# Optimization experiments

Hardware: AMD Instinct MI355X
Metric: run time of the kernel (lower is better)

## Reference

```python
import jax, jax.numpy as jnp
import numpy as np

B, C, H, N = 2, 128, 128, 2048   # batch, in_channels, hidden_dim, points per view
TEMP = 0.1
ITERS = 20
EPS = 1e-8


def setup_inputs() -> dict:
    key = jax.random.key(0)
    ks = jax.random.split(key, 4)
    s = lambda fan_in: 1.0 / np.sqrt(fan_in)
    return {
        "feat_d": jax.random.normal(ks[0], (B, C, N), jnp.float32),
        "feat_s": jax.random.normal(ks[1], (B, C, N), jnp.float32),
        # dustbin_head params: Conv1d(C->H, k=1) -> ReLU -> Conv1d(H->1, k=1)
        "W1": jax.random.normal(ks[2], (H, C), jnp.float32) * s(C),
        "b1": jnp.zeros((H,), jnp.float32),
        "W2": jax.random.normal(ks[3], (1, H), jnp.float32) * s(H),
        "b2": jnp.zeros((1,), jnp.float32),
    }


def _dustbin_head(x, W1, b1, W2, b2):
    # 1x1 Conv1d == channel matmul. x: [B, C, N] -> [B, 1, N]
    h = jax.nn.relu(jnp.einsum('hc,bcn->bhn', W1, x) + b1[None, :, None])
    return jnp.einsum('oh,bhn->bon', W2, h) + b2[None, :, None]


def _log_cross_view_ot(feat_q, feat_k, dustbin, temperature, iters):
    # scores: [B, Nq, Nk]; dustbin appended as the last row -> [B, Nq+1, Nk]
    scores = jnp.einsum('bcn,bcm->bnm', feat_q, feat_k) / temperature
    log_T0 = jnp.concatenate([scores, dustbin], axis=1)

    def step(log_T, _):
        log_T = log_T - jax.nn.logsumexp(log_T, axis=2, keepdims=True)  # row norm
        log_T = log_T - jax.nn.logsumexp(log_T, axis=1, keepdims=True)  # col norm
        return log_T, None

    log_T, _ = jax.lax.scan(step, log_T0, None, length=iters)
    return log_T


def reference(feat_d, feat_s, W1, b1, W2, b2):
    # N_d == N_s, so the torch F.interpolate calls are identity ops.
    dust_d = _dustbin_head(feat_d, W1, b1, W2, b2)  # [B, 1, N]
    dust_s = _dustbin_head(feat_s, W1, b1, W2, b2)  # [B, 1, N]

    log_T_ds = _log_cross_view_ot(feat_d, feat_s, dust_d, TEMP, ITERS)
    log_T_sd = _log_cross_view_ot(feat_s, feat_d, dust_s, TEMP, ITERS)

    T_ds = jnp.exp(log_T_ds[:, :-1, :])  # drop dustbin row -> [B, N, N]
    T_sd = jnp.exp(log_T_sd[:, :-1, :])

    loss_consistency = jnp.mean((T_ds - jnp.swapaxes(T_sd, 1, 2)) ** 2)

    entropy_ds = -(T_ds * jnp.log(T_ds + EPS)).sum(axis=(1, 2)).mean()
    entropy_sd = -(T_sd * jnp.log(T_sd + EPS)).sum(axis=(1, 2)).mean()
    loss_entropy = 0.5 * (entropy_ds + entropy_sd)

    return loss_consistency + 0.01 * loss_entropy
```

## Files before the change

kernel.cpp:

```cpp
#include <hip/hip_runtime.h>
#include <hip/hip_fp16.h>
#include <math.h>

#define NPTS 2048
#define NB 2
#define NC 128
#define NH 128
#define INV_TEMP 10.0f
#define NITERS 20
#define EPSF 1e-8f

static __device__ __forceinline__ void lse_merge(float& m, float& s, float m2, float s2){
  float M = fmaxf(m, m2);
  s = s * __expf(m - M) + s2 * __expf(m2 - M);
  m = M;
}

static __device__ __forceinline__ void unpack8(uint4 raw, float* x){
  float2 f;
  f = __half22float2(*(__half2*)&raw.x); x[0]=f.x; x[1]=f.y;
  f = __half22float2(*(((__half2*)&raw.x)+1)); x[2]=f.x; x[3]=f.y;
  f = __half22float2(*(__half2*)&raw.z); x[4]=f.x; x[5]=f.y;
  f = __half22float2(*(((__half2*)&raw.z)+1)); x[6]=f.x; x[7]=f.y;
}

static __device__ __forceinline__ float reduce32_lse(float* x){
  float m = x[0];
  #pragma unroll
  for (int i = 1; i < 32; ++i) m = fmaxf(m, x[i]);
  float s = 0.f;
  #pragma unroll
  for (int i = 0; i < 32; ++i) s += __expf(x[i] - m);
  #pragma unroll
  for (int d = 1; d < 64; d <<= 1){
    float m2 = __shfl_xor(m, d);
    float s2 = __shfl_xor(s, d);
    lse_merge(m, s, m2, s2);
  }
  return m + __logf(s);
}

__global__ __launch_bounds__(128) void dust_kernel(
    const float* __restrict__ fd, const float* __restrict__ fs,
    const float* __restrict__ W1, const float* __restrict__ b1,
    const float* __restrict__ W2, const float* __restrict__ b2,
    float* __restrict__ dust_d, float* __restrict__ dust_s){
  const int chunk = blockIdx.x, b = blockIdx.y, view = blockIdx.z;
  const float* x = (view == 0 ? fd : fs) + (size_t)b * NC * NPTS;
  float* out = (view == 0 ? dust_d : dust_s) + (size_t)b * NPTS;
  const int n0 = chunk * 16;
  __shared__ float xs[NC][17];
  __shared__ float red[NH][17];
  const int j = threadIdx.x;
  #pragma unroll
  for (int p = 0; p < 16; ++p) xs[j][p] = x[(size_t)j * NPTS + n0 + p];
  __syncthreads();
  float acc[16];
  float bb = b1[j];
  #pragma unroll
  for (int p = 0; p < 16; ++p) acc[p] = bb;
  for (int c = 0; c < NC; ++c){
    float w = W1[j * NC + c];
    #pragma unroll
    for (int p = 0; p < 16; ++p) acc[p] = fmaf(w, xs[c][p], acc[p]);
  }
  float w2 = W2[j];
  #pragma unroll
  for (int p = 0; p < 16; ++p) red[j][p] = w2 * fmaxf(acc[p], 0.0f);
  __syncthreads();
  for (int s = NH / 2; s >= 1; s >>= 1){
    if (j < s){
      #pragma unroll
      for (int p = 0; p < 16; ++p) red[j][p] += red[j + s][p];
    }
    __syncthreads();
  }
  if (j < 16) out[n0 + j] = red[0][j] + b2[0];
}

#define GP 68
__global__ __launch_bounds__(256) void gemm_kernel(
    const float* __restrict__ fd, const float* __restrict__ fs,
    __half* __restrict__ S, __half* __restrict__ ST){
  const int cb = blockIdx.x, rb = blockIdx.y, b = blockIdx.z;
  const float* A = fd + (size_t)b * NC * NPTS;
  const float* Bm = fs + (size_t)b * NC * NPTS;
  __shared__ float Als[NC * GP];
  __shared__ float Bls[NC * GP];
  const int tid = threadIdx.x;
  for (int idx = tid; idx < NC * 64; idx += 256){
    int ch = idx >> 6, i = idx & 63;
    Als[ch * GP + i] = A[(size_t)ch * NPTS + rb * 64 + i];
    Bls[ch * GP + i] = Bm[(size_t)ch * NPTS + cb * 64 + i];
  }
  __syncthreads();
  const int tx = tid & 15, ty = tid >> 4;
  float acc[4][4] = {};
  for (int c = 0; c < NC; ++c){
    float4 a4 = *(const float4*)&Als[c * GP + ty * 4];
    float4 b4 = *(const float4*)&Bls[c * GP + tx * 4];
    float av[4] = {a4.x, a4.y, a4.z, a4.w};
    float bv[4] = {b4.x, b4.y, b4.z, b4.w};
    #pragma unroll
    for (int i = 0; i < 4; ++i)
      #pragma unroll
      for (int jj = 0; jj < 4; ++jj)
        acc[i][jj] = fmaf(av[i], bv[jj], acc[i][jj]);
  }
  __half* Sb = S + (size_t)b * NPTS * NPTS;
  __half* STb = ST + (size_t)b * NPTS * NPTS;
  const int r0 = rb * 64 + ty * 4, c0 = cb * 64 + tx * 4;
  #pragma unroll
  for (int i = 0; i < 4; ++i){
    __half2 p[2];
    p[0] = __float22half2_rn(make_float2(acc[i][0]*INV_TEMP, acc[i][1]*INV_TEMP));
    p[1] = __float22half2_rn(make_float2(acc[i][2]*INV_TEMP, acc[i][3]*INV_TEMP));
    *(uint2*)&Sb[(size_t)(r0 + i) * NPTS + c0] = *(uint2*)p;
  }
  #pragma unroll
  for (int jj = 0; jj < 4; ++jj){
    __half2 p[2];
    p[0] = __float22half2_rn(make_float2(acc[0][jj]*INV_TEMP, acc[1][jj]*INV_TEMP));
    p[1] = __float22half2_rn(make_float2(acc[2][jj]*INV_TEMP, acc[3][jj]*INV_TEMP));
    *(uint2*)&STb[(size_t)(c0 + jj) * NPTS + r0] = *(uint2*)p;
  }
}

__global__ __launch_bounds__(512, 4) void phase_kernel(
    const __half* __restrict__ S, const __half* __restrict__ ST,
    const float* __restrict__ dust_d, const float* __restrict__ dust_s,
    float* __restrict__ u_ds, float* __restrict__ u_sd,
    float* __restrict__ v_ds, float* __restrict__ v_sd,
    const int mode){
  const int b = blockIdx.y, mat = blockIdx.z;
  const int w = threadIdx.x >> 6, lane = threadIdx.x & 63;
  const int r = blockIdx.x * 8 + w;
  const int rmax = (mode == 0) ? (NPTS + 1) : NPTS;

  __shared__ float lds_off[NPTS];
  {
    const float* off;
    if (mode == 0) off = (mat == 0 ? v_ds : v_sd) + b * NPTS;
    else           off = (mat == 0 ? u_sd : u_ds) + b * (NPTS + 1);
    *(float4*)&lds_off[threadIdx.x * 4] = *(const float4*)&off[threadIdx.x * 4];
  }
  __syncthreads();

  if (r >= rmax) return;

  float x[32];
  if (mode == 0 && r == NPTS){
    const float* drow = (mat == 0 ? dust_d : dust_s) + b * NPTS;
    #pragma unroll
    for (int k = 0; k < 8; ++k){
      const int c = (k * 64 + lane) * 4;
      float4 rv = *(const float4*)&drow[c];
      float4 o  = *(const float4*)&lds_off[c];
      x[k*4+0]=rv.x+o.x; x[k*4+1]=rv.y+o.y; x[k*4+2]=rv.z+o.z; x[k*4+3]=rv.w+o.w;
    }
  } else {
    const __half* row = ((mode == 0) == (mat == 0) ? S : ST);
    row = (mat == 0 ? S : ST);
    row += ((size_t)b * NPTS + r) * NPTS;
    #pragma unroll
    for (int k2 = 0; k2 < 4; ++k2){
      const int c = (k2 * 64 + lane) * 8;
      uint4 raw = *(const uint4*)&row[c];
      float xr[8];
      unpack8(raw, xr);
      float4 o0 = *(const float4*)&lds_off[c];
      float4 o1 = *(const float4*)&lds_off[c + 4];
      x[k2*8+0]=xr[0]+o0.x; x[k2*8+1]=xr[1]+o0.y; x[k2*8+2]=xr[2]+o0.z; x[k2*8+3]=xr[3]+o0.w;
      x[k2*8+4]=xr[4]+o1.x; x[k2*8+5]=xr[5]+o1.y; x[k2*8+6]=xr[6]+o1.z; x[k2*8+7]=xr[7]+o1.w;
    }
  }

  float lse = reduce32_lse(x);
  if (lane == 0){
    if (mode == 0){
      (mat == 0 ? u_ds : u_sd)[b * (NPTS + 1) + r] = -lse;
    } else {
      float dsc = (mat == 0 ? dust_s : dust_d)[b * NPTS + r];
      float uN  = (mat == 0 ? u_sd : u_ds)[b * (NPTS + 1) + NPTS];
      float e = dsc + uN;
      float M2 = fmaxf(lse, e);
      lse = M2 + __logf(__expf(lse - M2) + __expf(e - M2));
      (mat == 0 ? v_sd : v_ds)[b * NPTS + r] = -lse;
    }
  }
}

__global__ __launch_bounds__(512, 4) void loss_kernel(
    const __half* __restrict__ S,
    const float* __restrict__ u_ds, const float* __restrict__ u_sd,
    const float* __restrict__ v_ds, const float* __restrict__ v_sd,
    float* __restrict__ part){
  const int b = blockIdx.y;
  const int w = threadIdx.x >> 6, lane = threadIdx.x & 63;
  const int r = blockIdx.x * 8 + w;

  __shared__ float lds_vds[NPTS];
  __shared__ float lds_usd[NPTS];
  *(float4*)&lds_vds[threadIdx.x * 4] = *(const float4*)&v_ds[b * NPTS + threadIdx.x * 4];
  *(float4*)&lds_usd[threadIdx.x * 4] = *(const float4*)&u_sd[b * (NPTS + 1) + threadIdx.x * 4];
  __syncthreads();

  const __half* row = S + ((size_t)b * NPTS + r) * NPTS;
  const float uds = u_ds[b * (NPTS + 1) + r];
  const float vsd = v_sd[b * NPTS + r];
  float sd = 0.f, e1 = 0.f, e2 = 0.f;
  #pragma unroll
  for (int k2 = 0; k2 < 4; ++k2){
    const int c = (k2 * 64 + lane) * 8;
    uint4 raw = *(const uint4*)&row[c];
    float sv[8];
    unpack8(raw, sv);
    float4 a0 = *(const float4*)&lds_vds[c];
    float4 a1 = *(const float4*)&lds_vds[c + 4];
    float4 q0 = *(const float4*)&lds_usd[c];
    float4 q1 = *(const float4*)&lds_usd[c + 4];
    float av[8] = {a0.x,a0.y,a0.z,a0.w,a1.x,a1.y,a1.z,a1.w};
    float qv[8] = {q0.x,q0.y,q0.z,q0.w,q1.x,q1.y,q1.z,q1.w};
    #pragma unroll
    for (int i = 0; i < 8; ++i){
      float t1 = __expf(sv[i] + uds + av[i]);
      float t2 = __expf(sv[i] + qv[i] + vsd);
      float d = t1 - t2;
      sd += d * d;
      e1 += t1 * __logf(t1 + EPSF);
      e2 += t2 * __logf(t2 + EPSF);
    }
  }
  #pragma unroll
  for (int d = 1; d < 64; d <<= 1){
    sd += __shfl_xor(sd, d);
    e1 += __shfl_xor(e1, d);
    e2 += __shfl_xor(e2, d);
  }
  if (lane == 0){
    float* p = part + ((size_t)b * NPTS + r) * 4;
    p[0] = sd; p[1] = e1; p[2] = e2;
  }
}

__global__ __launch_bounds__(256) void final_kernel(const float* __restrict__ part, float* __restrict__ out){
  const int tid = threadIdx.x;
  float s0 = 0.f, s1 = 0.f, s2 = 0.f;
  for (int i = tid; i < NB * NPTS; i += 256){
    s0 += part[(size_t)i * 4 + 0];
    s1 += part[(size_t)i * 4 + 1];
    s2 += part[(size_t)i * 4 + 2];
  }
  #pragma unroll
  for (int d = 1; d < 64; d <<= 1){
    s0 += __shfl_xor(s0, d);
    s1 += __shfl_xor(s1, d);
    s2 += __shfl_xor(s2, d);
  }
  __shared__ float rs[4][3];
  const int w = tid >> 6;
  if ((tid & 63) == 0){ rs[w][0] = s0; rs[w][1] = s1; rs[w][2] = s2; }
  __syncthreads();
  if (tid == 0){
    float a0 = rs[0][0] + rs[1][0] + rs[2][0] + rs[3][0];
    float a1 = rs[0][1] + rs[1][1] + rs[2][1] + rs[3][1];
    float a2 = rs[0][2] + rs[1][2] + rs[2][2] + rs[3][2];
    float lc = a0 / (float)((size_t)NB * NPTS * NPTS);
    float le = -0.5f * (a1 + a2) / (float)NB;
    out[0] = lc + 0.01f * le;
  }
}

extern "C" void kernel_launch(void* const* d_in, const int* in_sizes, int n_in,
                              void* d_out, int out_size, void* d_ws, size_t ws_size,
                              hipStream_t stream){
  const float* fd = (const float*)d_in[0];
  const float* fs = (const float*)d_in[1];
  const float* W1 = (const float*)d_in[2];
  const float* b1 = (const float*)d_in[3];
  const float* W2 = (const float*)d_in[4];
  const float* b2 = (const float*)d_in[5];
  char* ws = (char*)d_ws;
  __half* S  = (__half*)ws;
  __half* ST = S + (size_t)NB * NPTS * NPTS;
  float* fws = (float*)(ws + 2 * sizeof(__half) * (size_t)NB * NPTS * NPTS);
  float* dust_d = fws;
  float* dust_s = dust_d + (size_t)NB * NPTS;
  float* u_ds   = dust_s + (size_t)NB * NPTS;
  float* u_sd   = u_ds + (size_t)NB * (NPTS + 1);
  float* v_ds   = u_sd + (size_t)NB * (NPTS + 1);
  float* v_sd   = v_ds + (size_t)NB * NPTS;
  float* part   = v_sd + (size_t)NB * NPTS;

  hipMemsetAsync(v_ds, 0, sizeof(float) * (size_t)NB * NPTS * 2, stream);

  dust_kernel<<<dim3(NPTS / 16, NB, 2), 128, 0, stream>>>(fd, fs, W1, b1, W2, b2, dust_d, dust_s);
  gemm_kernel<<<dim3(NPTS / 64, NPTS / 64, NB), 256, 0, stream>>>(fd, fs, S, ST);
  for (int it = 0; it < NITERS; ++it){
    phase_kernel<<<dim3((NPTS + 1 + 7) / 8, NB, 2), 512, 0, stream>>>(S, ST, dust_d, dust_s, u_ds, u_sd, v_ds, v_sd, 0);
    phase_kernel<<<dim3(NPTS / 8, NB, 2), 512, 0, stream>>>(S, ST, dust_d, dust_s, u_ds, u_sd, v_ds, v_sd, 1);
  }
  loss_kernel<<<dim3(NPTS / 8, NB), 512, 0, stream>>>(S, u_ds, u_sd, v_ds, v_sd, part);
  final_kernel<<<1, 256, 0, stream>>>(part, (float*)d_out);
}
```

Measured before the change: 398.4 us.

## Tree-reduce LSE max, split GEMM K into chunks, unify phase grid

The row log-sum-exp now finds its max with a pairwise tree and sums exponentials into four independent accumulators, which shortens the serial dependency chains. The GEMM loads K in two 64-channel chunks, halving its shared memory (about 68KB down to 34KB) so more blocks can be resident, at the cost of an extra barrier pair per chunk. Both phase launches now share one grid size, and surplus blocks exit early. The change also drops a dead row-pointer computation.

```diff
diff --git a/kernel.cpp b/kernel.cpp
--- a/kernel.cpp
+++ b/kernel.cpp
@@ -25,17 +25,28 @@
 }
 
 static __device__ __forceinline__ float reduce32_lse(float* x){
-  float m = x[0];
-  #pragma unroll
-  for (int i = 1; i < 32; ++i) m = fmaxf(m, x[i]);
-  float s = 0.f;
-  #pragma unroll
-  for (int i = 0; i < 32; ++i) s += __expf(x[i] - m);
+  float mt[16];
+  #pragma unroll
+  for (int i = 0; i < 16; ++i) mt[i] = fmaxf(x[i], x[i + 16]);
+  #pragma unroll
+  for (int st = 8; st >= 1; st >>= 1)
+    #pragma unroll
+    for (int i = 0; i < 8; ++i) if (i < st) mt[i] = fmaxf(mt[i], mt[i + st]);
+  float m = mt[0];
+  float s0 = 0.f, s1 = 0.f, s2 = 0.f, s3 = 0.f;
+  #pragma unroll
+  for (int i = 0; i < 32; i += 4){
+    s0 += __expf(x[i]     - m);
+    s1 += __expf(x[i + 1] - m);
+    s2 += __expf(x[i + 2] - m);
+    s3 += __expf(x[i + 3] - m);
+  }
+  float s = (s0 + s1) + (s2 + s3);
   #pragma unroll
   for (int d = 1; d < 64; d <<= 1){
     float m2 = __shfl_xor(m, d);
-    float s2 = __shfl_xor(s, d);
-    lse_merge(m, s, m2, s2);
+    float sx = __shfl_xor(s, d);
+    lse_merge(m, s, m2, sx);
   }
   return m + __logf(s);
 }
@@ -79,33 +90,37 @@
 }
 
 #define GP 68
+#define KC 64
 __global__ __launch_bounds__(256) void gemm_kernel(
     const float* __restrict__ fd, const float* __restrict__ fs,
     __half* __restrict__ S, __half* __restrict__ ST){
   const int cb = blockIdx.x, rb = blockIdx.y, b = blockIdx.z;
   const float* A = fd + (size_t)b * NC * NPTS;
   const float* Bm = fs + (size_t)b * NC * NPTS;
-  __shared__ float Als[NC * GP];
-  __shared__ float Bls[NC * GP];
+  __shared__ float Als[KC * GP];
+  __shared__ float Bls[KC * GP];
   const int tid = threadIdx.x;
-  for (int idx = tid; idx < NC * 64; idx += 256){
-    int ch = idx >> 6, i = idx & 63;
-    Als[ch * GP + i] = A[(size_t)ch * NPTS + rb * 64 + i];
-    Bls[ch * GP + i] = Bm[(size_t)ch * NPTS + cb * 64 + i];
-  }
-  __syncthreads();
   const int tx = tid & 15, ty = tid >> 4;
   float acc[4][4] = {};
-  for (int c = 0; c < NC; ++c){
-    float4 a4 = *(const float4*)&Als[c * GP + ty * 4];
-    float4 b4 = *(const float4*)&Bls[c * GP + tx * 4];
-    float av[4] = {a4.x, a4.y, a4.z, a4.w};
-    float bv[4] = {b4.x, b4.y, b4.z, b4.w};
-    #pragma unroll
-    for (int i = 0; i < 4; ++i)
+  for (int kc = 0; kc < NC; kc += KC){
+    for (int idx = tid; idx < KC * 64; idx += 256){
+      int ch = idx >> 6, i = idx & 63;
+      Als[ch * GP + i] = A[(size_t)(kc + ch) * NPTS + rb * 64 + i];
+      Bls[ch * GP + i] = Bm[(size_t)(kc + ch) * NPTS + cb * 64 + i];
+    }
+    __syncthreads();
+    for (int c = 0; c < KC; ++c){
+      float4 a4 = *(const float4*)&Als[c * GP + ty * 4];
+      float4 b4 = *(const float4*)&Bls[c * GP + tx * 4];
+      float av[4] = {a4.x, a4.y, a4.z, a4.w};
+      float bv[4] = {b4.x, b4.y, b4.z, b4.w};
       #pragma unroll
-      for (int jj = 0; jj < 4; ++jj)
-        acc[i][jj] = fmaf(av[i], bv[jj], acc[i][jj]);
+      for (int i = 0; i < 4; ++i)
+        #pragma unroll
+        for (int jj = 0; jj < 4; ++jj)
+          acc[i][jj] = fmaf(av[i], bv[jj], acc[i][jj]);
+    }
+    __syncthreads();
   }
   __half* Sb = S + (size_t)b * NPTS * NPTS;
   __half* STb = ST + (size_t)b * NPTS * NPTS;
@@ -136,6 +151,7 @@
   const int w = threadIdx.x >> 6, lane = threadIdx.x & 63;
   const int r = blockIdx.x * 8 + w;
   const int rmax = (mode == 0) ? (NPTS + 1) : NPTS;
+  if (blockIdx.x * 8 >= rmax) return;
 
   __shared__ float lds_off[NPTS];
   {
@@ -159,9 +175,7 @@
       x[k*4+0]=rv.x+o.x; x[k*4+1]=rv.y+o.y; x[k*4+2]=rv.z+o.z; x[k*4+3]=rv.w+o.w;
     }
   } else {
-    const __half* row = ((mode == 0) == (mat == 0) ? S : ST);
-    row = (mat == 0 ? S : ST);
-    row += ((size_t)b * NPTS + r) * NPTS;
+    const __half* row = (mat == 0 ? S : ST) + ((size_t)b * NPTS + r) * NPTS;
     #pragma unroll
     for (int k2 = 0; k2 < 4; ++k2){
       const int c = (k2 * 64 + lane) * 8;
@@ -296,9 +310,10 @@
 
   dust_kernel<<<dim3(NPTS / 16, NB, 2), 128, 0, stream>>>(fd, fs, W1, b1, W2, b2, dust_d, dust_s);
   gemm_kernel<<<dim3(NPTS / 64, NPTS / 64, NB), 256, 0, stream>>>(fd, fs, S, ST);
+  const dim3 pgrid((NPTS + 1 + 7) / 8, NB, 2);
   for (int it = 0; it < NITERS; ++it){
-    phase_kernel<<<dim3((NPTS + 1 + 7) / 8, NB, 2), 512, 0, stream>>>(S, ST, dust_d, dust_s, u_ds, u_sd, v_ds, v_sd, 0);
-    phase_kernel<<<dim3(NPTS / 8, NB, 2), 512, 0, stream>>>(S, ST, dust_d, dust_s, u_ds, u_sd, v_ds, v_sd, 1);
+    phase_kernel<<<pgrid, 512, 0, stream>>>(S, ST, dust_d, dust_s, u_ds, u_sd, v_ds, v_sd, 0);
+    phase_kernel<<<pgrid, 512, 0, stream>>>(S, ST, dust_d, dust_s, u_ds, u_sd, v_ds, v_sd, 1);
   }
   loss_kernel<<<dim3(NPTS / 8, NB), 512, 0, stream>>>(S, u_ds, u_sd, v_ds, v_sd, part);
   final_kernel<<<1, 256, 0, stream>>>(part, (float*)d_out);
```

Result: no change. 395.9 us (-0.6%).
